# Kernel optimization log

Measured on AMD Instinct MI355X. Metric: run time of the kernel, lower is better.

## Reference

```python
import jax, jax.numpy as jnp
import numpy as np

N_NODES = 100000
N_EDGES = 1600000
NFEAT = 256
NHID = 128


def setup_inputs() -> dict:
    key = jax.random.key(0)
    k1, k2, k3, k4, k5 = jax.random.split(key, 5)
    x = jax.random.normal(k1, (N_NODES, NFEAT), dtype=jnp.float32)
    edge_src = jax.random.randint(k2, (N_EDGES,), 0, N_NODES, dtype=jnp.int64)
    edge_dst = jax.random.randint(k3, (N_EDGES,), 0, N_NODES, dtype=jnp.int64)
    edge_w = jax.random.uniform(k4, (N_EDGES,), dtype=jnp.float32)
    W = jax.random.normal(k5, (NFEAT, NHID), dtype=jnp.float32) * (1.0 / np.sqrt(NFEAT))
    b = jnp.zeros((NHID,), dtype=jnp.float32)
    return {"x": x, "edge_src": edge_src, "edge_dst": edge_dst, "edge_w": edge_w, "W": W, "b": b}


def reference(x, edge_src, edge_dst, edge_w, W, b):
    # GraphConvolution: support = x @ W ; out = spmm(adj, support) + b ; then ReLU
    support = x @ W                                  # [N, nhid]
    msgs = support[edge_src] * edge_w[:, None]       # [E, nhid] gather + scale
    agg = jax.ops.segment_sum(msgs, edge_dst, num_segments=N_NODES)  # [N, nhid]
    return jax.nn.relu(agg + b)
```

## Files before the change

### kernel.cpp

```cpp
#include <hip/hip_runtime.h>
#include <hip/hip_bf16.h>

#define NFEAT 256
#define NHID  128
#define NPB   128
#define BMAX  2048

typedef short s16x8 __attribute__((ext_vector_type(8)));
typedef float f32x4 __attribute__((ext_vector_type(4)));
typedef float f32x2 __attribute__((ext_vector_type(2)));

static __device__ __forceinline__ ushort bfbits(float f) {
  __hip_bfloat16 h = __float2bfloat16(f);
  return *reinterpret_cast<ushort*>(&h);
}

__global__ __launch_bounds__(256) void wcvt_kernel(
    const float* __restrict__ W, ushort* __restrict__ Wt) {
  const int id = blockIdx.x * 256 + threadIdx.x;
  const int k = id >> 7, n = id & 127;
  Wt[n * NFEAT + k] = bfbits(W[id]);
}

__global__ __launch_bounds__(256) void hist_kernel(
    const int* __restrict__ edst, int* __restrict__ histT,
    int n_edges, int B, int G, int chunk) {
  __shared__ int hist[BMAX];
  const int g = blockIdx.x;
  for (int b = threadIdx.x; b < B; b += 256) hist[b] = 0;
  __syncthreads();
  const int e0 = g * chunk;
  const int e1 = (e0 + chunk < n_edges) ? e0 + chunk : n_edges;
  for (int e = e0 + threadIdx.x; e < e1; e += 256)
    atomicAdd(&hist[(uint)edst[e] >> 7], 1);
  __syncthreads();
  for (int b = threadIdx.x; b < B; b += 256) histT[(size_t)b * G + g] = hist[b];
}

__global__ __launch_bounds__(256) void scan1_kernel(
    const int* __restrict__ in, int* __restrict__ exc,
    int* __restrict__ bsums, int n) {
  const int tid = threadIdx.x;
  const int lane = tid & 63, wid = tid >> 6;
  const int base = blockIdx.x * 1024 + tid * 4;
  int v0 = 0, v1 = 0, v2 = 0, v3 = 0;
  if (base + 3 < n) {
    int4 v = *(const int4*)(in + base);
    v0 = v.x; v1 = v.y; v2 = v.z; v3 = v.w;
  } else {
    if (base + 0 < n) v0 = in[base + 0];
    if (base + 1 < n) v1 = in[base + 1];
    if (base + 2 < n) v2 = in[base + 2];
  }
  const int tsum = v0 + v1 + v2 + v3;
  int t = tsum;
#pragma unroll
  for (int d = 1; d < 64; d <<= 1) {
    int u = __shfl_up(t, d);
    if (lane >= d) t += u;
  }
  __shared__ int wtot[4], wpre[4];
  if (lane == 63) wtot[wid] = t;
  __syncthreads();
  if (tid == 0) {
    int s = 0;
    for (int w = 0; w < 4; ++w) { wpre[w] = s; s += wtot[w]; }
    bsums[blockIdx.x] = s;
  }
  __syncthreads();
  const int off = (t - tsum) + wpre[wid];
  if (base + 0 < n) exc[base + 0] = off;
  if (base + 1 < n) exc[base + 1] = off + v0;
  if (base + 2 < n) exc[base + 2] = off + v0 + v1;
  if (base + 3 < n) exc[base + 3] = off + v0 + v1 + v2;
}

__global__ __launch_bounds__(256) void scan2_kernel(int* __restrict__ bsums, int nb) {
  const int tid = threadIdx.x;
  const int lane = tid & 63, wid = tid >> 6;
  const int v = (tid < nb) ? bsums[tid] : 0;
  int t = v;
#pragma unroll
  for (int d = 1; d < 64; d <<= 1) {
    int u = __shfl_up(t, d);
    if (lane >= d) t += u;
  }
  __shared__ int wtot[4], wpre[4];
  if (lane == 63) wtot[wid] = t;
  __syncthreads();
  if (tid == 0) {
    int s = 0;
    for (int w = 0; w < 4; ++w) { wpre[w] = s; s += wtot[w]; }
  }
  __syncthreads();
  const int exc = (t - v) + wpre[wid];
  if (tid < nb) bsums[tid] = exc;
}

__global__ __launch_bounds__(256) void scan3_kernel(
    int* __restrict__ exc, const int* __restrict__ bsums,
    int* __restrict__ bucket_start, int n, int G, int B, int n_edges) {
  const int i = blockIdx.x * 256 + threadIdx.x;
  if (i < n) {
    const int v = exc[i] + bsums[i >> 10];
    exc[i] = v;
    if (i % G == 0) bucket_start[i / G] = v;
  }
  if (i == 0) bucket_start[B] = n_edges;
}

__global__ __launch_bounds__(256) void gemm_scatter_fused(
    const float* __restrict__ x, const ushort* __restrict__ Wt,
    ushort* __restrict__ sup, int n_nodes,
    const int* __restrict__ esrc, const int* __restrict__ edst,
    const float* __restrict__ ew, const int* __restrict__ base,
    int2* __restrict__ packed2, int n_edges, int B, int G, int chunk,
    int n_gemm) {
  __shared__ ushort As[64 * 64];
  __shared__ ushort Bs[128 * 64];

  const int idx = blockIdx.x;
  const long long total = (long long)n_gemm + G;
  const int c_lo = (int)((long long)idx * G / total);
  const int c_hi = (int)(((long long)idx + 1) * G / total);
  int role, sub;
  if (c_hi > c_lo) { role = 0; sub = c_lo; }
  else             { role = 1; sub = idx - c_hi; }

  if (role == 0) {
    int* cursor = (int*)As;
    const int g = sub;
    for (int b = threadIdx.x; b < B; b += 256) cursor[b] = base[(size_t)b * G + g];
    __syncthreads();
    const int e0 = g * chunk;
    const int e1 = (e0 + chunk < n_edges) ? e0 + chunk : n_edges;
    for (int e = e0 + threadIdx.x; e < e1; e += 256) {
      const int dst = edst[e];
      const int src = esrc[e];
      const float w = ew[e];
      const int pos = atomicAdd(&cursor[(uint)dst >> 7], 1);
      packed2[pos] = make_int2(src | ((dst & (NPB - 1)) << 18), __float_as_int(w));
    }
    return;
  }

  const int t = threadIdx.x;
  const int wid = t >> 6;
  const int lane = t & 63;
  const int rowBase = sub * 64;
  if (rowBase >= n_nodes) return;

  f32x4 acc[4][2];
#pragma unroll
  for (int m = 0; m < 4; ++m)
#pragma unroll
    for (int n = 0; n < 2; ++n) acc[m][n] = (f32x4){0.f, 0.f, 0.f, 0.f};

  const float4* x4 = (const float4*)x;

  for (int kc = 0; kc < 4; ++kc) {
    __syncthreads();
#pragma unroll
    for (int it = 0; it < 4; ++it) {
      const int i4 = t + it * 256;
      const int r = i4 >> 4, k4 = i4 & 15;
      const int row = rowBase + r;
      float4 v = make_float4(0.f, 0.f, 0.f, 0.f);
      if (row < n_nodes) v = x4[(size_t)row * (NFEAT / 4) + kc * 16 + k4];
      ushort4 h;
      h.x = bfbits(v.x); h.y = bfbits(v.y); h.z = bfbits(v.z); h.w = bfbits(v.w);
      int byte = (r << 7) + (k4 << 3);
      byte ^= (r & 7) << 4;
      *(ushort4*)((char*)As + byte) = h;
    }
#pragma unroll
    for (int it = 0; it < 8; ++it) {
      const int i2 = t + it * 256;
      const int col = i2 >> 4, k4 = i2 & 15;
      const ushort4 h = *(const ushort4*)(Wt + col * NFEAT + kc * 64 + k4 * 4);
      int byte = (col << 7) + (k4 << 3);
      byte ^= (col & 7) << 4;
      *(ushort4*)((char*)Bs + byte) = h;
    }
    __syncthreads();
#pragma unroll
    for (int ks = 0; ks < 2; ++ks) {
      const int k0 = ks * 32 + (lane >> 4) * 8;
      s16x8 af[4], bfr[2];
#pragma unroll
      for (int m = 0; m < 4; ++m) {
        const int r = m * 16 + (lane & 15);
        int byte = (r << 7) + (k0 << 1);
        byte ^= (r & 7) << 4;
        af[m] = *(const s16x8*)((const char*)As + byte);
      }
#pragma unroll
      for (int n = 0; n < 2; ++n) {
        const int c = wid * 32 + n * 16 + (lane & 15);
        int byte = (c << 7) + (k0 << 1);
        byte ^= (c & 7) << 4;
        bfr[n] = *(const s16x8*)((const char*)Bs + byte);
      }
#pragma unroll
      for (int m = 0; m < 4; ++m)
#pragma unroll
        for (int n = 0; n < 2; ++n)
          acc[m][n] = __builtin_amdgcn_mfma_f32_16x16x32_bf16(af[m], bfr[n], acc[m][n], 0, 0, 0);
    }
  }

#pragma unroll
  for (int m = 0; m < 4; ++m) {
#pragma unroll
    for (int rr = 0; rr < 4; ++rr) {
      const int row = rowBase + m * 16 + (lane >> 4) * 4 + rr;
      if (row < n_nodes) {
#pragma unroll
        for (int n = 0; n < 2; ++n) {
          const int col = wid * 32 + n * 16 + (lane & 15);
          sup[(size_t)row * NHID + col] = bfbits(acc[m][n][rr]);
        }
      }
    }
  }
}

__global__ __launch_bounds__(256) void bucket_build_kernel(
    const int2* __restrict__ packed2, const int* __restrict__ bucket_start,
    int2* __restrict__ packedN, int* __restrict__ row_start,
    int n_nodes, int n_edges) {
  __shared__ int cnt[NPB];
  __shared__ int st[NPB];
  __shared__ int cur[NPB];
  __shared__ int w0tot;
  const int tid = threadIdx.x;
  const int b = blockIdx.x;
  const int s0 = bucket_start[b];
  const int s1 = bucket_start[b + 1];
  const int m = s1 - s0;

  if (tid < NPB) cnt[tid] = 0;
  __syncthreads();

  for (int i = tid; i < m; i += 256)
    atomicAdd(&cnt[((uint)packed2[s0 + i].x >> 18) & (NPB - 1)], 1);
  __syncthreads();

  {
    const int v = (tid < NPB) ? cnt[tid] : 0;
    int t = v;
#pragma unroll
    for (int d = 1; d < 64; d <<= 1) {
      int u = __shfl_up(t, d);
      if ((tid & 63) >= d) t += u;
    }
    if (tid == 63) w0tot = t;
    __syncthreads();
    if (tid < NPB) {
      const int s = (t - v) + ((tid >= 64) ? w0tot : 0);
      st[tid] = s;
      cur[tid] = s;
    }
    __syncthreads();
  }

  for (int i = tid; i < m; i += 256) {
    const int2 e = packed2[s0 + i];
    const int dl = ((uint)e.x >> 18) & (NPB - 1);
    const int pos = atomicAdd(&cur[dl], 1);
    packedN[s0 + pos] = e;
  }

  if (tid < NPB) {
    const int node = b * NPB + tid;
    if (node < n_nodes) row_start[node] = s0 + st[tid];
  }
  if (b == 0 && tid == 0) row_start[n_nodes] = n_edges;
}

__global__ __launch_bounds__(256) void agg_kernel(
    const ushort* __restrict__ sup, const int2* __restrict__ packed,
    const int* __restrict__ row_start, const float* __restrict__ bias,
    float* __restrict__ out, int n_nodes) {
  const int node = blockIdx.x * 4 + (threadIdx.x >> 6);
  if (node >= n_nodes) return;
  const int lane = threadIdx.x & 63;
  const int start = __builtin_amdgcn_readfirstlane(row_start[node]);
  const int end   = __builtin_amdgcn_readfirstlane(row_start[node + 1]);

  float a0 = 0.f, a1 = 0.f, b0 = 0.f, b1 = 0.f;
  float c0 = 0.f, c1 = 0.f, d0 = 0.f, d1 = 0.f;
  int i = start;
  for (; i + 7 < end; i += 8) {
    const int2 e0 = packed[i + 0];
    const int2 e1 = packed[i + 1];
    const int2 e2 = packed[i + 2];
    const int2 e3 = packed[i + 3];
    const int2 e4 = packed[i + 4];
    const int2 e5 = packed[i + 5];
    const int2 e6 = packed[i + 6];
    const int2 e7 = packed[i + 7];
    const uint u0 = *(const uint*)(sup + ((size_t)((uint)e0.x & 0x3FFFFu) << 7) + lane * 2);
    const uint u1 = *(const uint*)(sup + ((size_t)((uint)e1.x & 0x3FFFFu) << 7) + lane * 2);
    const uint u2 = *(const uint*)(sup + ((size_t)((uint)e2.x & 0x3FFFFu) << 7) + lane * 2);
    const uint u3 = *(const uint*)(sup + ((size_t)((uint)e3.x & 0x3FFFFu) << 7) + lane * 2);
    const uint u4 = *(const uint*)(sup + ((size_t)((uint)e4.x & 0x3FFFFu) << 7) + lane * 2);
    const uint u5 = *(const uint*)(sup + ((size_t)((uint)e5.x & 0x3FFFFu) << 7) + lane * 2);
    const uint u6 = *(const uint*)(sup + ((size_t)((uint)e6.x & 0x3FFFFu) << 7) + lane * 2);
    const uint u7 = *(const uint*)(sup + ((size_t)((uint)e7.x & 0x3FFFFu) << 7) + lane * 2);
    const float w0 = __int_as_float(e0.y), w1 = __int_as_float(e1.y);
    const float w2 = __int_as_float(e2.y), w3 = __int_as_float(e3.y);
    const float w4 = __int_as_float(e4.y), w5 = __int_as_float(e5.y);
    const float w6 = __int_as_float(e6.y), w7 = __int_as_float(e7.y);
    a0 += __uint_as_float(u0 << 16) * w0 + __uint_as_float(u4 << 16) * w4;
    a1 += __uint_as_float(u0 & 0xffff0000u) * w0 + __uint_as_float(u4 & 0xffff0000u) * w4;
    b0 += __uint_as_float(u1 << 16) * w1 + __uint_as_float(u5 << 16) * w5;
    b1 += __uint_as_float(u1 & 0xffff0000u) * w1 + __uint_as_float(u5 & 0xffff0000u) * w5;
    c0 += __uint_as_float(u2 << 16) * w2 + __uint_as_float(u6 << 16) * w6;
    c1 += __uint_as_float(u2 & 0xffff0000u) * w2 + __uint_as_float(u6 & 0xffff0000u) * w6;
    d0 += __uint_as_float(u3 << 16) * w3 + __uint_as_float(u7 << 16) * w7;
    d1 += __uint_as_float(u3 & 0xffff0000u) * w3 + __uint_as_float(u7 & 0xffff0000u) * w7;
  }
  for (; i + 3 < end; i += 4) {
    const int2 e0 = packed[i + 0];
    const int2 e1 = packed[i + 1];
    const int2 e2 = packed[i + 2];
    const int2 e3 = packed[i + 3];
    const uint u0 = *(const uint*)(sup + ((size_t)((uint)e0.x & 0x3FFFFu) << 7) + lane * 2);
    const uint u1 = *(const uint*)(sup + ((size_t)((uint)e1.x & 0x3FFFFu) << 7) + lane * 2);
    const uint u2 = *(const uint*)(sup + ((size_t)((uint)e2.x & 0x3FFFFu) << 7) + lane * 2);
    const uint u3 = *(const uint*)(sup + ((size_t)((uint)e3.x & 0x3FFFFu) << 7) + lane * 2);
    const float w0 = __int_as_float(e0.y), w1 = __int_as_float(e1.y);
    const float w2 = __int_as_float(e2.y), w3 = __int_as_float(e3.y);
    a0 += __uint_as_float(u0 << 16) * w0 + __uint_as_float(u2 << 16) * w2;
    a1 += __uint_as_float(u0 & 0xffff0000u) * w0 + __uint_as_float(u2 & 0xffff0000u) * w2;
    b0 += __uint_as_float(u1 << 16) * w1 + __uint_as_float(u3 << 16) * w3;
    b1 += __uint_as_float(u1 & 0xffff0000u) * w1 + __uint_as_float(u3 & 0xffff0000u) * w3;
  }
  for (; i < end; ++i) {
    const int2 e0 = packed[i];
    const uint u0 = *(const uint*)(sup + ((size_t)((uint)e0.x & 0x3FFFFu) << 7) + lane * 2);
    const float w0 = __int_as_float(e0.y);
    a0 += __uint_as_float(u0 << 16) * w0;
    a1 += __uint_as_float(u0 & 0xffff0000u) * w0;
  }

  const float2 bb = ((const float2*)bias)[lane];
  f32x2 r;
  r.x = fmaxf((a0 + b0) + (c0 + d0) + bb.x, 0.f);
  r.y = fmaxf((a1 + b1) + (c1 + d1) + bb.y, 0.f);
  __builtin_nontemporal_store(r, (f32x2*)out + (size_t)node * (NHID / 2) + lane);
}

__global__ __launch_bounds__(256) void scatter_bf16_kernel(
    const ushort* __restrict__ sup, const int* __restrict__ esrc,
    const int* __restrict__ edst, const float* __restrict__ ew,
    float* __restrict__ out, int n_edges) {
  const long long idx = (long long)blockIdx.x * 256 + threadIdx.x;
  const int e = (int)(idx >> 6);
  const int c2 = (int)(idx & 63);
  if (e >= n_edges) return;
  const int s = esrc[e];
  const int d = edst[e];
  const float wt = ew[e];
  const uint u = *(const uint*)(sup + (size_t)s * NHID + c2 * 2);
  float* drow = out + (size_t)d * NHID + c2 * 2;
  atomicAdd(drow + 0, __uint_as_float(u << 16) * wt);
  atomicAdd(drow + 1, __uint_as_float(u & 0xffff0000u) * wt);
}

__global__ __launch_bounds__(256) void bias_relu_kernel(
    float* __restrict__ out, const float* __restrict__ b, int n4) {
  const int i = blockIdx.x * 256 + threadIdx.x;
  if (i >= n4) return;
  float4 v = ((float4*)out)[i];
  const float4 bb = ((const float4*)b)[i & (NHID / 4 - 1)];
  v.x = fmaxf(v.x + bb.x, 0.f);
  v.y = fmaxf(v.y + bb.y, 0.f);
  v.z = fmaxf(v.z + bb.z, 0.f);
  v.w = fmaxf(v.w + bb.w, 0.f);
  ((float4*)out)[i] = v;
}

static inline size_t align_up(size_t v, size_t a) { return (v + a - 1) & ~(a - 1); }

extern "C" void kernel_launch(void* const* d_in, const int* in_sizes, int n_in,
                              void* d_out, int out_size, void* d_ws, size_t ws_size,
                              hipStream_t stream) {
  const float* x    = (const float*)d_in[0];
  const int*   esrc = (const int*)d_in[1];
  const int*   edst = (const int*)d_in[2];
  const float* ew   = (const float*)d_in[3];
  const float* W    = (const float*)d_in[4];
  const float* b    = (const float*)d_in[5];
  float* out = (float*)d_out;

  const int n_nodes = in_sizes[0] / NFEAT;
  const int n_edges = in_sizes[1];

  const int B = (n_nodes + NPB - 1) / NPB;
  int G = (n_edges + 8191) / 8192;
  const int Gmax = (256 * 1024) / (B > 0 ? B : 1);
  if (G > Gmax) G = Gmax;
  if (G < 1) G = 1;
  const int chunk = (int)align_up((size_t)(n_edges + G - 1) / G, 256);
  G = (n_edges + chunk - 1) / chunk;

  char* ws = (char*)d_ws;
  size_t off = 0;
  ushort* sup       = (ushort*)(ws + off); off = align_up(off + (size_t)n_nodes * NHID * 2, 256);
  ushort* Wt        = (ushort*)(ws + off); off = align_up(off + (size_t)NFEAT * NHID * 2, 256);
  int* histT        = (int*)(ws + off);    off = align_up(off + (size_t)B * G * 4, 256);
  int* exc          = (int*)(ws + off);    off = align_up(off + (size_t)B * G * 4, 256);
  int* bsums        = (int*)(ws + off);    off = align_up(off + 1024 * 4, 256);
  int* bucket_start = (int*)(ws + off);    off = align_up(off + ((size_t)B + 1) * 4, 256);
  int* row_start    = (int*)(ws + off);    off = align_up(off + ((size_t)n_nodes + 1) * 4, 256);
  int2* packed2     = (int2*)(ws + off);   off = align_up(off + (size_t)n_edges * 8, 256);
  int2* packedN     = (int2*)(ws + off);   off = align_up(off + (size_t)n_edges * 8, 256);
  const bool csr_ok = (off <= ws_size) && (n_nodes <= 256 * 1024) && (B <= BMAX);

  const int n_gemm = (n_nodes + 63) / 64;

  if (csr_ok) {
    wcvt_kernel<<<(NFEAT * NHID) / 256, 256, 0, stream>>>(W, Wt);

    hist_kernel<<<G, 256, 0, stream>>>(edst, histT, n_edges, B, G, chunk);

    const int n_scan = B * G;
    const int nb = (n_scan + 1023) / 1024;
    scan1_kernel<<<nb, 256, 0, stream>>>(histT, exc, bsums, n_scan);
    scan2_kernel<<<1, 256, 0, stream>>>(bsums, nb);
    scan3_kernel<<<(n_scan + 255) / 256, 256, 0, stream>>>(exc, bsums, bucket_start, n_scan, G, B, n_edges);

    gemm_scatter_fused<<<n_gemm + G, 256, 0, stream>>>(
        x, Wt, sup, n_nodes, esrc, edst, ew, exc, packed2,
        n_edges, B, G, chunk, n_gemm);

    bucket_build_kernel<<<B, 256, 0, stream>>>(
        packed2, bucket_start, packedN, row_start, n_nodes, n_edges);

    agg_kernel<<<(n_nodes + 3) / 4, 256, 0, stream>>>(sup, packedN, row_start, b, out, n_nodes);
  } else {
    wcvt_kernel<<<(NFEAT * NHID) / 256, 256, 0, stream>>>(W, Wt);
    gemm_scatter_fused<<<n_gemm, 256, 0, stream>>>(
        x, Wt, sup, n_nodes, esrc, edst, ew, (int*)d_ws, (int2*)d_ws,
        0, 1, 0, 1, n_gemm);
    hipMemsetAsync(out, 0, (size_t)n_nodes * NHID * sizeof(float), stream);
    const long long threads = (long long)n_edges * 64;
    scatter_bf16_kernel<<<(int)((threads + 255) / 256), 256, 0, stream>>>(sup, esrc, edst, ew, out, n_edges);
    const int n4 = n_nodes * NHID / 4;
    bias_relu_kernel<<<(n4 + 255) / 256, 256, 0, stream>>>(out, b, n4);
  }
}
```

Baseline: 146.5 us.

## Shrink scatter chunks, merge W conversion into histogram, transpose bucket offsets

Fixes the edge chunk size at 2048, so there are many more histogram and scatter blocks (G grows from about 196 to 782). The W bf16 conversion now runs inside the histogram kernel, which removes one launch. scan3 writes the per-chunk bucket bases transposed, so each scatter block reads its cursors contiguously. The scatter loads 8 edges per thread up front before issuing the atomics. The cost is a scan array about four times larger and a scan2 that loops serially over more block sums.

```diff
diff --git a/kernel.cpp b/kernel.cpp
--- a/kernel.cpp
+++ b/kernel.cpp
@@ -5,6 +5,7 @@
 #define NHID  128
 #define NPB   128
 #define BMAX  2048
+#define SCHUNK 2048
 
 typedef short s16x8 __attribute__((ext_vector_type(8)));
 typedef float f32x4 __attribute__((ext_vector_type(4)));
@@ -15,22 +16,22 @@
   return *reinterpret_cast<ushort*>(&h);
 }
 
-__global__ __launch_bounds__(256) void wcvt_kernel(
-    const float* __restrict__ W, ushort* __restrict__ Wt) {
-  const int id = blockIdx.x * 256 + threadIdx.x;
-  const int k = id >> 7, n = id & 127;
-  Wt[n * NFEAT + k] = bfbits(W[id]);
-}
-
-__global__ __launch_bounds__(256) void hist_kernel(
+__global__ __launch_bounds__(256) void prep_kernel(
+    const float* __restrict__ W, ushort* __restrict__ Wt,
     const int* __restrict__ edst, int* __restrict__ histT,
-    int n_edges, int B, int G, int chunk) {
+    int n_edges, int B, int G) {
   __shared__ int hist[BMAX];
-  const int g = blockIdx.x;
+  if (blockIdx.x < 128) {
+    const int id = blockIdx.x * 256 + threadIdx.x;
+    const int k = id >> 7, n = id & 127;
+    Wt[n * NFEAT + k] = bfbits(W[id]);
+    return;
+  }
+  const int g = blockIdx.x - 128;
   for (int b = threadIdx.x; b < B; b += 256) hist[b] = 0;
   __syncthreads();
-  const int e0 = g * chunk;
-  const int e1 = (e0 + chunk < n_edges) ? e0 + chunk : n_edges;
+  const int e0 = g * SCHUNK;
+  const int e1 = (e0 + SCHUNK < n_edges) ? e0 + SCHUNK : n_edges;
   for (int e = e0 + threadIdx.x; e < e1; e += 256)
     atomicAdd(&hist[(uint)edst[e] >> 7], 1);
   __syncthreads();
@@ -76,35 +77,43 @@
 }
 
 __global__ __launch_bounds__(256) void scan2_kernel(int* __restrict__ bsums, int nb) {
+  __shared__ int wtot[4], wpre[4], tot_s;
   const int tid = threadIdx.x;
   const int lane = tid & 63, wid = tid >> 6;
-  const int v = (tid < nb) ? bsums[tid] : 0;
-  int t = v;
-#pragma unroll
-  for (int d = 1; d < 64; d <<= 1) {
-    int u = __shfl_up(t, d);
-    if (lane >= d) t += u;
-  }
-  __shared__ int wtot[4], wpre[4];
-  if (lane == 63) wtot[wid] = t;
-  __syncthreads();
-  if (tid == 0) {
-    int s = 0;
-    for (int w = 0; w < 4; ++w) { wpre[w] = s; s += wtot[w]; }
-  }
-  __syncthreads();
-  const int exc = (t - v) + wpre[wid];
-  if (tid < nb) bsums[tid] = exc;
+  int carry = 0;
+  for (int base = 0; base < nb; base += 256) {
+    const int idx = base + tid;
+    const int v = (idx < nb) ? bsums[idx] : 0;
+    int t = v;
+#pragma unroll
+    for (int d = 1; d < 64; d <<= 1) {
+      int u = __shfl_up(t, d);
+      if (lane >= d) t += u;
+    }
+    if (lane == 63) wtot[wid] = t;
+    __syncthreads();
+    if (tid == 0) {
+      int s = 0;
+      for (int w = 0; w < 4; ++w) { wpre[w] = s; s += wtot[w]; }
+      tot_s = s;
+    }
+    __syncthreads();
+    if (idx < nb) bsums[idx] = carry + (t - v) + wpre[wid];
+    carry += tot_s;
+    __syncthreads();
+  }
 }
 
 __global__ __launch_bounds__(256) void scan3_kernel(
-    int* __restrict__ exc, const int* __restrict__ bsums,
-    int* __restrict__ bucket_start, int n, int G, int B, int n_edges) {
+    const int* __restrict__ exc, const int* __restrict__ bsums,
+    int* __restrict__ baseT, int* __restrict__ bucket_start,
+    int n, int G, int B, int n_edges) {
   const int i = blockIdx.x * 256 + threadIdx.x;
   if (i < n) {
     const int v = exc[i] + bsums[i >> 10];
-    exc[i] = v;
-    if (i % G == 0) bucket_start[i / G] = v;
+    const int b = i / G, g = i % G;
+    baseT[(size_t)g * B + b] = v;
+    if (g == 0) bucket_start[b] = v;
   }
   if (i == 0) bucket_start[B] = n_edges;
 }
@@ -113,9 +122,8 @@
     const float* __restrict__ x, const ushort* __restrict__ Wt,
     ushort* __restrict__ sup, int n_nodes,
     const int* __restrict__ esrc, const int* __restrict__ edst,
-    const float* __restrict__ ew, const int* __restrict__ base,
-    int2* __restrict__ packed2, int n_edges, int B, int G, int chunk,
-    int n_gemm) {
+    const float* __restrict__ ew, const int* __restrict__ baseT,
+    int2* __restrict__ packed2, int n_edges, int B, int G, int n_gemm) {
   __shared__ ushort As[64 * 64];
   __shared__ ushort Bs[128 * 64];
 
@@ -130,16 +138,28 @@
   if (role == 0) {
     int* cursor = (int*)As;
     const int g = sub;
-    for (int b = threadIdx.x; b < B; b += 256) cursor[b] = base[(size_t)b * G + g];
-    __syncthreads();
-    const int e0 = g * chunk;
-    const int e1 = (e0 + chunk < n_edges) ? e0 + chunk : n_edges;
-    for (int e = e0 + threadIdx.x; e < e1; e += 256) {
-      const int dst = edst[e];
-      const int src = esrc[e];
-      const float w = ew[e];
-      const int pos = atomicAdd(&cursor[(uint)dst >> 7], 1);
-      packed2[pos] = make_int2(src | ((dst & (NPB - 1)) << 18), __float_as_int(w));
+    for (int b = threadIdx.x; b < B; b += 256) cursor[b] = baseT[(size_t)g * B + b];
+    __syncthreads();
+    const int e0 = g * SCHUNK;
+    if (e0 + SCHUNK <= n_edges) {
+      int d[8], s[8]; float w[8];
+#pragma unroll
+      for (int j = 0; j < 8; ++j) {
+        const int e = e0 + j * 256 + threadIdx.x;
+        d[j] = edst[e]; s[j] = esrc[e]; w[j] = ew[e];
+      }
+#pragma unroll
+      for (int j = 0; j < 8; ++j) {
+        const int pos = atomicAdd(&cursor[(uint)d[j] >> 7], 1);
+        packed2[pos] = make_int2(s[j] | ((d[j] & (NPB - 1)) << 18), __float_as_int(w[j]));
+      }
+    } else {
+      const int e1 = n_edges;
+      for (int e = e0 + threadIdx.x; e < e1; e += 256) {
+        const int dst = edst[e];
+        const int pos = atomicAdd(&cursor[(uint)dst >> 7], 1);
+        packed2[pos] = make_int2(esrc[e] | ((dst & (NPB - 1)) << 18), __float_as_int(ew[e]));
+      }
     }
     return;
   }
@@ -399,12 +419,8 @@
   const int n_edges = in_sizes[1];
 
   const int B = (n_nodes + NPB - 1) / NPB;
-  int G = (n_edges + 8191) / 8192;
-  const int Gmax = (256 * 1024) / (B > 0 ? B : 1);
-  if (G > Gmax) G = Gmax;
-  if (G < 1) G = 1;
-  const int chunk = (int)align_up((size_t)(n_edges + G - 1) / G, 256);
-  G = (n_edges + chunk - 1) / chunk;
+  const int G = (n_edges + SCHUNK - 1) / SCHUNK;
+  const long long n_scan_ll = (long long)B * G;
 
   char* ws = (char*)d_ws;
   size_t off = 0;
@@ -412,39 +428,38 @@
   ushort* Wt        = (ushort*)(ws + off); off = align_up(off + (size_t)NFEAT * NHID * 2, 256);
   int* histT        = (int*)(ws + off);    off = align_up(off + (size_t)B * G * 4, 256);
   int* exc          = (int*)(ws + off);    off = align_up(off + (size_t)B * G * 4, 256);
+  int* baseT        = (int*)(ws + off);    off = align_up(off + (size_t)B * G * 4, 256);
   int* bsums        = (int*)(ws + off);    off = align_up(off + 1024 * 4, 256);
   int* bucket_start = (int*)(ws + off);    off = align_up(off + ((size_t)B + 1) * 4, 256);
   int* row_start    = (int*)(ws + off);    off = align_up(off + ((size_t)n_nodes + 1) * 4, 256);
   int2* packed2     = (int2*)(ws + off);   off = align_up(off + (size_t)n_edges * 8, 256);
   int2* packedN     = (int2*)(ws + off);   off = align_up(off + (size_t)n_edges * 8, 256);
-  const bool csr_ok = (off <= ws_size) && (n_nodes <= 256 * 1024) && (B <= BMAX);
+  const bool csr_ok = (off <= ws_size) && (n_nodes <= 256 * 1024) && (B <= BMAX) &&
+                      (n_scan_ll <= 1024 * 1024);
 
   const int n_gemm = (n_nodes + 63) / 64;
 
   if (csr_ok) {
-    wcvt_kernel<<<(NFEAT * NHID) / 256, 256, 0, stream>>>(W, Wt);
-
-    hist_kernel<<<G, 256, 0, stream>>>(edst, histT, n_edges, B, G, chunk);
-
-    const int n_scan = B * G;
+    prep_kernel<<<128 + G, 256, 0, stream>>>(W, Wt, edst, histT, n_edges, B, G);
+
+    const int n_scan = (int)n_scan_ll;
     const int nb = (n_scan + 1023) / 1024;
     scan1_kernel<<<nb, 256, 0, stream>>>(histT, exc, bsums, n_scan);
     scan2_kernel<<<1, 256, 0, stream>>>(bsums, nb);
-    scan3_kernel<<<(n_scan + 255) / 256, 256, 0, stream>>>(exc, bsums, bucket_start, n_scan, G, B, n_edges);
+    scan3_kernel<<<(n_scan + 255) / 256, 256, 0, stream>>>(exc, bsums, baseT, bucket_start, n_scan, G, B, n_edges);
 
     gemm_scatter_fused<<<n_gemm + G, 256, 0, stream>>>(
-        x, Wt, sup, n_nodes, esrc, edst, ew, exc, packed2,
-        n_edges, B, G, chunk, n_gemm);
+        x, Wt, sup, n_nodes, esrc, edst, ew, baseT, packed2, n_edges, B, G, n_gemm);
 
     bucket_build_kernel<<<B, 256, 0, stream>>>(
         packed2, bucket_start, packedN, row_start, n_nodes, n_edges);
 
     agg_kernel<<<(n_nodes + 3) / 4, 256, 0, stream>>>(sup, packedN, row_start, b, out, n_nodes);
   } else {
-    wcvt_kernel<<<(NFEAT * NHID) / 256, 256, 0, stream>>>(W, Wt);
+    prep_kernel<<<128, 256, 0, stream>>>(W, Wt, edst, (int*)d_ws, 0, 1, 1);
     gemm_scatter_fused<<<n_gemm, 256, 0, stream>>>(
         x, Wt, sup, n_nodes, esrc, edst, ew, (int*)d_ws, (int2*)d_ws,
-        0, 1, 0, 1, n_gemm);
+        0, 1, 0, n_gemm);
     hipMemsetAsync(out, 0, (size_t)n_nodes * NHID * sizeof(float), stream);
     const long long threads = (long long)n_edges * 64;
     scatter_bf16_kernel<<<(int)((threads + 255) / 256), 256, 0, stream>>>(sup, esrc, edst, ew, out, n_edges);
```

Measured after the change: 139.2 us (median of 2 runs). -5.0%, faster.
